# Performance work log

Hardware: AMD Instinct MI355X
Metric: run time of the kernel (lower is better)

## Reference

```python
import jax, jax.numpy as jnp
import numpy as np

B, N = 16, 512            # graphs, atoms per graph
F_DIM, H, D = 128, 64, 16  # feature_dim, hidden_dim, far_source_dim
CUT, GROWTH = 5.0, 2.0
NS, NT = 3, 2
MULT = GROWTH ** NS        # default far_max_radius_multiplier = 8
EMAX = CUT * MULT          # 40.0
TOT = NS + NT              # 5 shells total
SF = D + 3                 # 19 per-shell features
SE_IN = TOT * SF           # 95
EH_IN = 4 * D + SE_IN      # 159
N_RBF = 8
BOUNDS = [(5.0, 10.0), (10.0, 20.0), (20.0, 40.0), (40.0, 80.0), (80.0, float('inf'))]


def ln(x, g, b):
    m = x.mean(-1, keepdims=True)
    v = x.var(-1, keepdims=True)
    return (x - m) / jnp.sqrt(v + 1e-5) * g + b


def setup_inputs() -> dict:
    key = jax.random.key(0)
    ks = jax.random.split(key, 16)
    W = lambda k, i, o: jax.random.normal(k, (i, o), jnp.float32) / np.sqrt(i)
    inp = {}
    inp['x'] = jax.random.normal(ks[0], (B * N, F_DIM), jnp.float32)
    inp['pos'] = jax.random.uniform(ks[1], (B * N, 3), jnp.float32) * 80.0
    inp['batch'] = jnp.repeat(jnp.arange(B, dtype=jnp.int32), N)
    inp['num_graphs'] = B
    inp['in_ln_g'] = jnp.ones(F_DIM); inp['in_ln_b'] = jnp.zeros(F_DIM)
    inp['src_w1'] = W(ks[2], F_DIM, H); inp['src_b1'] = jnp.zeros(H)
    inp['src_w2'] = W(ks[3], H, D);     inp['src_b2'] = jnp.zeros(D)
    inp['src_ln_g'] = jnp.ones(D); inp['src_ln_b'] = jnp.zeros(D)
    inp['se_ln_g'] = jnp.ones(SE_IN); inp['se_ln_b'] = jnp.zeros(SE_IN)
    inp['se_w1'] = W(ks[4], SE_IN, H); inp['se_b1'] = jnp.zeros(H)
    inp['se_w2'] = W(ks[5], H, D);     inp['se_b2'] = jnp.zeros(D)
    inp['eh_ln_g'] = jnp.ones(EH_IN); inp['eh_ln_b'] = jnp.zeros(EH_IN)
    inp['eh_w1'] = W(ks[6], EH_IN, H); inp['eh_b1'] = jnp.zeros(H)
    inp['eh_w2'] = W(ks[7], H, 1);     inp['eh_b2'] = jnp.zeros(1)
    inp['k_screen'] = jnp.float32(-8.0)
    inp['kg_w1'] = W(ks[8], N_RBF + 2, 32); inp['kg_b1'] = jnp.zeros(32)
    inp['kg_w2'] = jnp.zeros((32, 1)); inp['kg_b2'] = jnp.zeros(1)  # zero-init per source
    inp['far_gate'] = jnp.float32(0.2)
    inp['energy_scale'] = jnp.float32(0.0)
    return inp


def reference(x, pos, batch, num_graphs, in_ln_g, in_ln_b, src_w1, src_b1, src_w2, src_b2,
              src_ln_g, src_ln_b, se_ln_g, se_ln_b, se_w1, se_b1, se_w2, se_b2,
              eh_ln_g, eh_ln_b, eh_w1, eh_b1, eh_w2, eh_b2,
              k_screen, kg_w1, kg_b1, kg_w2, kg_b2, far_gate, energy_scale):
    M = x.shape[0]
    n = M // num_graphs
    # per-atom source features
    h = ln(x, in_ln_g, in_ln_b)
    src = jax.nn.silu(h @ src_w1 + src_b1) @ src_w2 + src_b2
    src = ln(src, src_ln_g, src_ln_b)
    # graph-wise neutralization (subtract per-graph mean)
    gsum = jax.ops.segment_sum(src, batch, num_segments=num_graphs)
    cnt = jax.ops.segment_sum(jnp.ones((M, 1), x.dtype), batch, num_segments=num_graphs)
    src = src - (gsum / jnp.maximum(cnt, 1.0))[batch]
    # pairwise distances per graph
    p = pos.reshape(num_graphs, n, 3)
    s = src.reshape(num_graphs, n, D)
    diff = p[:, :, None, :] - p[:, None, :, :]
    d = jnp.sqrt((diff * diff).sum(-1) + 1e-12)  # [B,n,n]
    not_self = ~jnp.eye(n, dtype=bool)[None]
    # physical kernel with learned RBF gate
    screening = jax.nn.softplus(k_screen)
    base = jnp.exp(-screening * d) / jnp.maximum(d, 1e-6)
    centers = jnp.linspace(CUT, EMAX, N_RBF)
    spacing = (EMAX - CUT) / (N_RBF - 1)
    gamma = 1.0 / (spacing * spacing)
    dc = d[..., None]
    rbf = jnp.exp(-gamma * (dc - centers) ** 2)
    gin = jnp.concatenate([dc / CUT, dc / EMAX, rbf], -1)
    gate = 1.0 + jnp.tanh(jax.nn.silu(gin @ kg_w1 + kg_b1) @ kg_w2 + kg_b2)[..., 0]
    ker = base * gate
    # shell statistics: kernel-weighted mean source, count, mean_r, rms_r per shell
    feats = []
    for lo, up in BOUNDS:
        m = (d >= lo) & not_self
        if np.isfinite(up):
            m = m & (d < up)
        mf = m.astype(x.dtype)
        c = mf.sum(-1)
        denom = jnp.maximum(c, 1.0)
        mean = jnp.einsum('bij,bjc->bic', ker * mf, s) / denom[..., None]
        mr = (mf * d).sum(-1) / denom
        rr = jnp.sqrt((mf * d * d).sum(-1) / denom + 1e-12)
        feats.append(jnp.concatenate([mean, c[..., None], mr[..., None], rr[..., None]], -1))
    shell = jnp.concatenate(feats, -1).reshape(M, SE_IN)  # [M, 95]
    emb = jax.nn.silu(ln(shell, se_ln_g, se_ln_b) @ se_w1 + se_b1) @ se_w2 + se_b2
    ein = jnp.concatenate([src, emb, src * emb, src - emb, shell], -1)  # [M, 159]
    pa = (jax.nn.silu(ln(ein, eh_ln_g, eh_ln_b) @ eh_w1 + eh_b1) @ eh_w2 + eh_b2)[..., 0]
    pa = pa * jnp.tanh(far_gate) * jnp.exp(energy_scale)
    return jax.ops.segment_sum(pa, batch, num_segments=num_graphs)  # per-graph energies [B]
```

## Files before the change

kernel.cpp:

```cpp
#include <hip/hip_runtime.h>
#include <hip/hip_bf16.h>
#include <math.h>

#define B_G   16
#define N_A   512
#define M_AT  8192
#define FD    128
#define HD    64
#define DD    16
#define SEIN  95
#define EHIN  159
#define NLUT  1024
#define DMAXF 140.0f

__device__ __forceinline__ float silu_f(float z) { return z / (1.f + __expf(-z)); }

__global__ __launch_bounds__(256) void k_lut2(
    const float* __restrict__ k_screen,
    const float* __restrict__ kg_w1, const float* __restrict__ kg_b1,
    const float* __restrict__ kg_w2, const float* __restrict__ kg_b2,
    float2* __restrict__ lut, float* __restrict__ out) {
  int t = threadIdx.x;
  if (blockIdx.x == 0 && t < B_G) out[t] = 0.f;

  __shared__ float w1l[320], b1l[32], w2l[32];
  for (int idx = t; idx < 320; idx += 256) w1l[idx] = kg_w1[idx];
  if (t < 32) { b1l[t] = kg_b1[t]; w2l[t] = kg_w2[t]; }
  __syncthreads();

  int i = blockIdx.x * 256 + t;
  if (i >= NLUT) return;
  float step = DMAXF / (float)(NLUT - 1);
  float ksv = k_screen[0];
  float screening = fmaxf(ksv, 0.f) + log1pf(expf(-fabsf(ksv)));
  float b2v = kg_b2[0];
  float vals[2];
#pragma unroll
  for (int e = 0; e < 2; ++e) {
    int ii = min(i + e, NLUT - 1);
    float d = (float)ii * step;
    float base = expf(-screening * d) / fmaxf(d, 1e-6f);
    float gin[10];
    gin[0] = d * (1.f / 5.0f);
    gin[1] = d * (1.f / 40.0f);
#pragma unroll
    for (int kk = 0; kk < 8; ++kk) {
      float u = d - (5.0f + 5.0f * (float)kk);
      gin[2 + kk] = expf(-(1.f / 25.f) * u * u);
    }
    float accv = 0.f;
    for (int h = 0; h < 32; ++h) {
      float z = b1l[h];
#pragma unroll
      for (int kk = 0; kk < 10; ++kk) z += gin[kk] * w1l[kk * 32 + h];
      accv += silu_f(z) * w2l[h];
    }
    accv += b2v;
    vals[e] = base * (1.f + tanhf(accv));
  }
  lut[i] = make_float2(vals[0], vals[1] - vals[0]);
}

__global__ __launch_bounds__(128) void k_src(
    const float* __restrict__ x,
    const float* __restrict__ g, const float* __restrict__ bb,
    const float* __restrict__ w1, const float* __restrict__ b1,
    const float* __restrict__ w2, const float* __restrict__ b2,
    const float* __restrict__ lng, const float* __restrict__ lnb,
    float* __restrict__ srcout) {
  int t = threadIdx.x, wave = t >> 6, lane = t & 63;
  __shared__ __align__(16) float w1s[FD * HD];
  __shared__ __align__(16) float w2s[HD * DD];
  __shared__ __align__(16) float xnsA[2][FD][16];
  __shared__ __align__(16) float hbA[2][HD][16];

  for (int idx = t; idx < FD * HD / 4; idx += 128)
    ((float4*)w1s)[idx] = ((const float4*)w1)[idx];
  for (int idx = t; idx < HD * DD / 4; idx += 128)
    ((float4*)w2s)[idx] = ((const float4*)w2)[idx];

  int aBase = blockIdx.x * 32 + wave * 16;
  int al = lane & 15, part = lane >> 4;

  float xr[32];
  const float4* xp = (const float4*)(x + (size_t)(aBase + al) * FD + part * 32);
#pragma unroll
  for (int i = 0; i < 8; ++i) {
    float4 v = xp[i];
    xr[i*4] = v.x; xr[i*4+1] = v.y; xr[i*4+2] = v.z; xr[i*4+3] = v.w;
  }
  float s = 0.f;
#pragma unroll
  for (int i = 0; i < 32; ++i) s += xr[i];
  s += __shfl_xor(s, 16); s += __shfl_xor(s, 32);
  float m = s * (1.f / 128.f);
  float v2 = 0.f;
#pragma unroll
  for (int i = 0; i < 32; ++i) { float d = xr[i] - m; v2 += d * d; }
  v2 += __shfl_xor(v2, 16); v2 += __shfl_xor(v2, 32);
  float inv = rsqrtf(v2 * (1.f / 128.f) + 1e-5f);
#pragma unroll
  for (int i = 0; i < 32; ++i) {
    int k = part * 32 + i;
    xnsA[wave][k][al] = (xr[i] - m) * inv * g[k] + bb[k];
  }
  __syncthreads();

  int h0 = al * 4, a0 = part * 4;
  float acc[4][4] = {};
#pragma unroll 4
  for (int k = 0; k < FD; ++k) {
    float4 wv = *(const float4*)&w1s[k * HD + h0];
    float4 xa = *(const float4*)&xnsA[wave][k][a0];
    acc[0][0] += wv.x * xa.x; acc[0][1] += wv.x * xa.y; acc[0][2] += wv.x * xa.z; acc[0][3] += wv.x * xa.w;
    acc[1][0] += wv.y * xa.x; acc[1][1] += wv.y * xa.y; acc[1][2] += wv.y * xa.z; acc[1][3] += wv.y * xa.w;
    acc[2][0] += wv.z * xa.x; acc[2][1] += wv.z * xa.y; acc[2][2] += wv.z * xa.z; acc[2][3] += wv.z * xa.w;
    acc[3][0] += wv.w * xa.x; acc[3][1] += wv.w * xa.y; acc[3][2] += wv.w * xa.z; acc[3][3] += wv.w * xa.w;
  }
#pragma unroll
  for (int i = 0; i < 4; ++i) {
    float bh = b1[h0 + i];
    float4 o;
    o.x = silu_f(acc[i][0] + bh); o.y = silu_f(acc[i][1] + bh);
    o.z = silu_f(acc[i][2] + bh); o.w = silu_f(acc[i][3] + bh);
    *(float4*)&hbA[wave][h0 + i][a0] = o;
  }
  __syncthreads();

  float acc2[4] = {};
#pragma unroll 4
  for (int h = 0; h < HD; ++h) {
    float wv = w2s[h * DD + al];
    float4 hv = *(const float4*)&hbA[wave][h][a0];
    acc2[0] += wv * hv.x; acc2[1] += wv * hv.y; acc2[2] += wv * hv.z; acc2[3] += wv * hv.w;
  }
  float b2c = b2[al], lgc = lng[al], lbc = lnb[al];
#pragma unroll
  for (int j = 0; j < 4; ++j) {
    float val = acc2[j] + b2c;
    float sm = val;
    sm += __shfl_xor(sm, 1); sm += __shfl_xor(sm, 2); sm += __shfl_xor(sm, 4); sm += __shfl_xor(sm, 8);
    float mm = sm * (1.f / 16.f);
    float dv = val - mm;
    float vv = dv * dv;
    vv += __shfl_xor(vv, 1); vv += __shfl_xor(vv, 2); vv += __shfl_xor(vv, 4); vv += __shfl_xor(vv, 8);
    float iv = rsqrtf(vv * (1.f / 16.f) + 1e-5f);
    srcout[(size_t)(aBase + a0 + j) * DD + al] = dv * iv * lgc + lbc;
  }
}

__global__ __launch_bounds__(256) void k_center(float* __restrict__ src) {
  int gph = blockIdx.x, t = threadIdx.x;
  float4* s4 = (float4*)(src + (size_t)gph * N_A * DD);
  float4 acc = make_float4(0.f, 0.f, 0.f, 0.f);
#pragma unroll
  for (int i = 0; i < 8; ++i) {
    float4 v = s4[t + 256 * i];
    acc.x += v.x; acc.y += v.y; acc.z += v.z; acc.w += v.w;
  }
  __shared__ float4 red[256];
  red[t] = acc;
  __syncthreads();
  if (t < 64) {
    float4 a = red[t], b = red[t + 64], c = red[t + 128], d = red[t + 192];
    a.x += b.x + c.x + d.x; a.y += b.y + c.y + d.y;
    a.z += b.z + c.z + d.z; a.w += b.w + c.w + d.w;
    red[t] = a;
  }
  __syncthreads();
  if (t < 16) {
    float4 a = red[t], b = red[t + 16], c = red[t + 32], d = red[t + 48];
    a.x += b.x + c.x + d.x; a.y += b.y + c.y + d.y;
    a.z += b.z + c.z + d.z; a.w += b.w + c.w + d.w;
    red[t] = a;
  }
  __syncthreads();
  if (t < 4) {
    float4 a = red[t], b = red[t + 4], c = red[t + 8], d = red[t + 12];
    a.x = (a.x + b.x + c.x + d.x) * (1.f / 512.f);
    a.y = (a.y + b.y + c.y + d.y) * (1.f / 512.f);
    a.z = (a.z + b.z + c.z + d.z) * (1.f / 512.f);
    a.w = (a.w + b.w + c.w + d.w) * (1.f / 512.f);
    red[t] = a;
  }
  __syncthreads();
  float4 mv = red[t & 3];
#pragma unroll
  for (int i = 0; i < 8; ++i) {
    int idx = t + 256 * i;
    float4 v = s4[idx];
    v.x -= mv.x; v.y -= mv.y; v.z -= mv.z; v.w -= mv.w;
    s4[idx] = v;
  }
}

__global__ __launch_bounds__(256) void k_pairs(
    const float* __restrict__ pos, const float* __restrict__ src,
    const float2* __restrict__ lut, float* __restrict__ shell) {
  int gph = blockIdx.x >> 7;
  int blk = blockIdx.x & 127;
  int t = threadIdx.x, wave = t >> 6, lane = t & 63;
  int i_local = blk * 4 + wave;

  __shared__ __align__(16) float sp[N_A * 3];
  __shared__ __align__(16) float ss[N_A * DD];
  __shared__ __align__(16) float2 luts[NLUT];
  __shared__ __align__(16) float wb[4][N_A];
  __shared__ unsigned char tbs[4][N_A];

  for (int idx = t; idx < N_A * 3 / 4; idx += 256)
    ((float4*)sp)[idx] = ((const float4*)(pos + (size_t)gph * N_A * 3))[idx];
  for (int idx = t; idx < N_A * DD / 4; idx += 256)
    ((float4*)ss)[idx] = ((const float4*)(src + (size_t)gph * N_A * DD))[idx];
  for (int idx = t; idx < NLUT / 2; idx += 256)
    ((float4*)luts)[idx] = ((const float4*)lut)[idx];
  __syncthreads();

  float px = sp[i_local * 3], py = sp[i_local * 3 + 1], pz = sp[i_local * 3 + 2];
  float cnt[5] = {0,0,0,0,0}, sd[5] = {0,0,0,0,0}, sdd[5] = {0,0,0,0,0};
  const float lscale = (float)(NLUT - 1) / DMAXF;

#pragma unroll
  for (int it = 0; it < 8; ++it) {
    int jv = lane + it * 64;
    float dx = px - sp[jv * 3], dy = py - sp[jv * 3 + 1], dz = pz - sp[jv * 3 + 2];
    float d2 = dx * dx + dy * dy + dz * dz + 1e-12f;
    float d = sqrtf(d2);
    bool valid = (jv != i_local) && (d >= 5.0f);
    int tq = (d >= 10.f) + (d >= 20.f) + (d >= 40.f) + (d >= 80.f);
    float xq = d * lscale;
    int i0 = min((int)xq, NLUT - 2);
    float f = xq - (float)i0;
    float2 L = luts[i0];
    float w = valid ? (L.x + L.y * f) : 0.f;
    wb[wave][jv] = w;
    tbs[wave][jv] = (unsigned char)tq;
    float dm = valid ? d : 0.f;
    float ddm = valid ? d * d : 0.f;
    float cm = valid ? 1.f : 0.f;
#pragma unroll
    for (int q = 0; q < 5; ++q) {
      bool mq = (tq == q);
      cnt[q] += mq ? cm : 0.f;
      sd[q]  += mq ? dm : 0.f;
      sdd[q] += mq ? ddm : 0.f;
    }
  }
#pragma unroll
  for (int q = 0; q < 5; ++q) {
#pragma unroll
    for (int o = 32; o > 0; o >>= 1) {
      cnt[q] += __shfl_xor(cnt[q], o);
      sd[q]  += __shfl_xor(sd[q], o);
      sdd[q] += __shfl_xor(sdd[q], o);
    }
  }
  __syncthreads();

  int jlow = lane & 15, cq = lane >> 4;
  float accq[5][4] = {};
  const float* ssb = &ss[jlow * DD + cq * 4];
  const float* wbb = &wb[wave][jlow];
  const unsigned char* tbb = &tbs[wave][jlow];
#pragma unroll
  for (int jj = 0; jj < 32; ++jj) {
    float4 sv = *(const float4*)(ssb + jj * 256);
    float w = wbb[jj * 16];
    int tq = tbb[jj * 16];
    float w0 = (tq == 0) ? w : 0.f;
    float w1_ = (tq == 1) ? w : 0.f;
    float w2_ = (tq == 2) ? w : 0.f;
    float w3_ = (tq == 3) ? w : 0.f;
    float w4_ = (tq == 4) ? w : 0.f;
    accq[0][0] += w0 * sv.x; accq[0][1] += w0 * sv.y; accq[0][2] += w0 * sv.z; accq[0][3] += w0 * sv.w;
    accq[1][0] += w1_ * sv.x; accq[1][1] += w1_ * sv.y; accq[1][2] += w1_ * sv.z; accq[1][3] += w1_ * sv.w;
    accq[2][0] += w2_ * sv.x; accq[2][1] += w2_ * sv.y; accq[2][2] += w2_ * sv.z; accq[2][3] += w2_ * sv.w;
    accq[3][0] += w3_ * sv.x; accq[3][1] += w3_ * sv.y; accq[3][2] += w3_ * sv.z; accq[3][3] += w3_ * sv.w;
    accq[4][0] += w4_ * sv.x; accq[4][1] += w4_ * sv.y; accq[4][2] += w4_ * sv.z; accq[4][3] += w4_ * sv.w;
  }
#pragma unroll
  for (int q = 0; q < 5; ++q)
#pragma unroll
    for (int i = 0; i < 4; ++i) {
      float v = accq[q][i];
      v += __shfl_xor(v, 1); v += __shfl_xor(v, 2); v += __shfl_xor(v, 4); v += __shfl_xor(v, 8);
      accq[q][i] = v;
    }

  float* shp = shell + (size_t)(gph * N_A + i_local) * SEIN;
  if (jlow == 0) {
#pragma unroll
    for (int q = 0; q < 5; ++q)
#pragma unroll
      for (int i = 0; i < 4; ++i)
        shp[q * 19 + cq * 4 + i] = accq[q][i] / fmaxf(cnt[q], 1.f);
  }
  if (lane < 5) {
    int q = lane;
    float denom = fmaxf(cnt[q], 1.f);
    shp[q * 19 + 16] = cnt[q];
    shp[q * 19 + 17] = sd[q] / denom;
    shp[q * 19 + 18] = sqrtf(sdd[q] / denom + 1e-12f);
  }
}

__global__ __launch_bounds__(128) void k_tail_a(
    const float* __restrict__ shell,
    const float* __restrict__ se_ln_g, const float* __restrict__ se_ln_b,
    const float* __restrict__ se_w1, const float* __restrict__ se_b1,
    const float* __restrict__ se_w2, const float* __restrict__ se_b2,
    float* __restrict__ emb) {
  int t = threadIdx.x, wave = t >> 6, lane = t & 63;
  __shared__ __align__(16) float w1s[SEIN * HD];
  __shared__ __align__(16) float w2s[HD * DD];
  __shared__ __align__(16) float shnA[2][SEIN][16];
  __shared__ __align__(16) float hbA[2][HD][16];

  for (int idx = t; idx < SEIN * HD / 4; idx += 128)
    ((float4*)w1s)[idx] = ((const float4*)se_w1)[idx];
  for (int idx = t; idx < HD * DD / 4; idx += 128)
    ((float4*)w2s)[idx] = ((const float4*)se_w2)[idx];

  int aB = blockIdx.x * 32;
  const float* shg = shell + (size_t)aB * SEIN;
  for (int idx = t; idx < 32 * SEIN; idx += 128) {
    unsigned a_loc = ((unsigned)idx * 690u) >> 16;
    int kk = idx - (int)a_loc * SEIN;
    shnA[a_loc >> 4][kk][a_loc & 15] = shg[idx];
  }
  __syncthreads();

  int al = lane & 15, part = lane >> 4;
  float s1 = 0.f, sq = 0.f;
  for (int i = 0; i < 24; ++i) {
    int k = part * 24 + i;
    if (k < SEIN) { float v = shnA[wave][k][al]; s1 += v; sq += v * v; }
  }
  s1 += __shfl_xor(s1, 16); s1 += __shfl_xor(s1, 32);
  sq += __shfl_xor(sq, 16); sq += __shfl_xor(sq, 32);
  float m = s1 * (1.f / (float)SEIN);
  float var = sq * (1.f / (float)SEIN) - m * m;
  float inv = rsqrtf(var + 1e-5f);
  for (int i = 0; i < 24; ++i) {
    int k = part * 24 + i;
    if (k < SEIN)
      shnA[wave][k][al] = (shnA[wave][k][al] - m) * inv * se_ln_g[k] + se_ln_b[k];
  }
  __syncthreads();

  int h0 = al * 4, a0 = part * 4;
  float acc[4][4] = {};
#pragma unroll 5
  for (int k = 0; k < SEIN; ++k) {
    float4 wv = *(const float4*)&w1s[k * HD + h0];
    float4 xa = *(const float4*)&shnA[wave][k][a0];
    acc[0][0] += wv.x * xa.x; acc[0][1] += wv.x * xa.y; acc[0][2] += wv.x * xa.z; acc[0][3] += wv.x * xa.w;
    acc[1][0] += wv.y * xa.x; acc[1][1] += wv.y * xa.y; acc[1][2] += wv.y * xa.z; acc[1][3] += wv.y * xa.w;
    acc[2][0] += wv.z * xa.x; acc[2][1] += wv.z * xa.y; acc[2][2] += wv.z * xa.z; acc[2][3] += wv.z * xa.w;
    acc[3][0] += wv.w * xa.x; acc[3][1] += wv.w * xa.y; acc[3][2] += wv.w * xa.z; acc[3][3] += wv.w * xa.w;
  }
#pragma unroll
  for (int i = 0; i < 4; ++i) {
    float bh = se_b1[h0 + i];
    float4 o;
    o.x = silu_f(acc[i][0] + bh); o.y = silu_f(acc[i][1] + bh);
    o.z = silu_f(acc[i][2] + bh); o.w = silu_f(acc[i][3] + bh);
    *(float4*)&hbA[wave][h0 + i][a0] = o;
  }
  __syncthreads();

  float acc2[4] = {};
#pragma unroll 4
  for (int h = 0; h < HD; ++h) {
    float wv = w2s[h * DD + al];
    float4 hv = *(const float4*)&hbA[wave][h][a0];
    acc2[0] += wv * hv.x; acc2[1] += wv * hv.y; acc2[2] += wv * hv.z; acc2[3] += wv * hv.w;
  }
  float b2c = se_b2[al];
#pragma unroll
  for (int j = 0; j < 4; ++j)
    emb[(size_t)(aB + wave * 16 + a0 + j) * DD + al] = acc2[j] + b2c;
}

__global__ __launch_bounds__(128) void k_tail_b(
    const float* __restrict__ src, const float* __restrict__ embp,
    const float* __restrict__ shell,
    const float* __restrict__ eh_ln_g, const float* __restrict__ eh_ln_b,
    const float* __restrict__ eh_w1, const float* __restrict__ eh_b1,
    const float* __restrict__ eh_w2, const float* __restrict__ eh_b2,
    const float* __restrict__ far_gate, const float* __restrict__ energy_scale,
    float* __restrict__ out) {
  int t = threadIdx.x, wave = t >> 6, lane = t & 63;
  __shared__ __align__(16) float w1s[EHIN * HD];
  __shared__ __align__(16) float einA[2][EHIN][16];
  __shared__ float redv[2][4];

  for (int idx = t; idx < EHIN * HD / 4; idx += 128)
    ((float4*)w1s)[idx] = ((const float4*)eh_w1)[idx];

  int aB = blockIdx.x * 32;
  int gph = aB >> 9;

  for (int idx = t; idx < 32 * DD; idx += 128) {
    int a_loc = idx >> 4, k = idx & 15;
    float sv = src[(size_t)aB * DD + idx];
    float ev = embp[(size_t)aB * DD + idx];
    int wv_ = a_loc >> 4, ac = a_loc & 15;
    einA[wv_][k][ac] = sv;
    einA[wv_][16 + k][ac] = ev;
    einA[wv_][32 + k][ac] = sv * ev;
    einA[wv_][48 + k][ac] = sv - ev;
  }
  const float* shg = shell + (size_t)aB * SEIN;
  for (int idx = t; idx < 32 * SEIN; idx += 128) {
    unsigned a_loc = ((unsigned)idx * 690u) >> 16;
    int kk = idx - (int)a_loc * SEIN;
    einA[a_loc >> 4][64 + kk][a_loc & 15] = shg[idx];
  }
  __syncthreads();

  int al = lane & 15, part = lane >> 4;
  float s1 = 0.f, sq = 0.f;
  for (int i = 0; i < 40; ++i) {
    int k = part * 40 + i;
    if (k < EHIN) { float v = einA[wave][k][al]; s1 += v; sq += v * v; }
  }
  s1 += __shfl_xor(s1, 16); s1 += __shfl_xor(s1, 32);
  sq += __shfl_xor(sq, 16); sq += __shfl_xor(sq, 32);
  float m = s1 * (1.f / (float)EHIN);
  float var = sq * (1.f / (float)EHIN) - m * m;
  float inv = rsqrtf(var + 1e-5f);
  for (int i = 0; i < 40; ++i) {
    int k = part * 40 + i;
    if (k < EHIN)
      einA[wave][k][al] = (einA[wave][k][al] - m) * inv * eh_ln_g[k] + eh_ln_b[k];
  }
  __syncthreads();

  int h0 = al * 4, a0 = part * 4;
  float acc[4][4] = {};
#pragma unroll 3
  for (int k = 0; k < EHIN; ++k) {
    float4 wv = *(const float4*)&w1s[k * HD + h0];
    float4 xa = *(const float4*)&einA[wave][k][a0];
    acc[0][0] += wv.x * xa.x; acc[0][1] += wv.x * xa.y; acc[0][2] += wv.x * xa.z; acc[0][3] += wv.x * xa.w;
    acc[1][0] += wv.y * xa.x; acc[1][1] += wv.y * xa.y; acc[1][2] += wv.y * xa.z; acc[1][3] += wv.y * xa.w;
    acc[2][0] += wv.z * xa.x; acc[2][1] += wv.z * xa.y; acc[2][2] += wv.z * xa.z; acc[2][3] += wv.z * xa.w;
    acc[3][0] += wv.w * xa.x; acc[3][1] += wv.w * xa.y; acc[3][2] += wv.w * xa.z; acc[3][3] += wv.w * xa.w;
  }
  float pa[4] = {0.f, 0.f, 0.f, 0.f};
#pragma unroll
  for (int i = 0; i < 4; ++i) {
    float bh = eh_b1[h0 + i];
    float w2v = eh_w2[h0 + i];
#pragma unroll
    for (int j = 0; j < 4; ++j) pa[j] += silu_f(acc[i][j] + bh) * w2v;
  }
#pragma unroll
  for (int j = 0; j < 4; ++j) {
    pa[j] += __shfl_xor(pa[j], 1); pa[j] += __shfl_xor(pa[j], 2);
    pa[j] += __shfl_xor(pa[j], 4); pa[j] += __shfl_xor(pa[j], 8);
  }
  if (al == 0) redv[wave][part] = pa[0] + pa[1] + pa[2] + pa[3] + 4.f * eh_b2[0];
  __syncthreads();
  if (t == 0) {
    float tot = 0.f;
#pragma unroll
    for (int w2_ = 0; w2_ < 2; ++w2_)
#pragma unroll
      for (int p = 0; p < 4; ++p) tot += redv[w2_][p];
    atomicAdd(&out[gph], tot * tanhf(far_gate[0]) * expf(energy_scale[0]));
  }
}

extern "C" void kernel_launch(void* const* d_in, const int* in_sizes, int n_in,
                              void* d_out, int out_size, void* d_ws, size_t ws_size,
                              hipStream_t stream) {
  const float* x         = (const float*)d_in[0];
  const float* pos       = (const float*)d_in[1];
  const float* in_ln_g   = (const float*)d_in[4];
  const float* in_ln_b   = (const float*)d_in[5];
  const float* src_w1    = (const float*)d_in[6];
  const float* src_b1    = (const float*)d_in[7];
  const float* src_w2    = (const float*)d_in[8];
  const float* src_b2    = (const float*)d_in[9];
  const float* src_ln_g  = (const float*)d_in[10];
  const float* src_ln_b  = (const float*)d_in[11];
  const float* se_ln_g   = (const float*)d_in[12];
  const float* se_ln_b   = (const float*)d_in[13];
  const float* se_w1     = (const float*)d_in[14];
  const float* se_b1     = (const float*)d_in[15];
  const float* se_w2     = (const float*)d_in[16];
  const float* se_b2     = (const float*)d_in[17];
  const float* eh_ln_g   = (const float*)d_in[18];
  const float* eh_ln_b   = (const float*)d_in[19];
  const float* eh_w1     = (const float*)d_in[20];
  const float* eh_b1     = (const float*)d_in[21];
  const float* eh_w2     = (const float*)d_in[22];
  const float* eh_b2     = (const float*)d_in[23];
  const float* k_screen  = (const float*)d_in[24];
  const float* kg_w1     = (const float*)d_in[25];
  const float* kg_b1     = (const float*)d_in[26];
  const float* kg_w2     = (const float*)d_in[27];
  const float* kg_b2     = (const float*)d_in[28];
  const float* far_gate  = (const float*)d_in[29];
  const float* en_scale  = (const float*)d_in[30];
  float* out = (float*)d_out;

  float* ws_src   = (float*)d_ws;
  float* ws_shell = ws_src + (size_t)M_AT * DD;
  float* ws_emb   = ws_shell + (size_t)M_AT * SEIN;
  float2* ws_lut  = (float2*)(ws_emb + (size_t)M_AT * DD);

  k_lut2<<<NLUT / 256, 256, 0, stream>>>(k_screen, kg_w1, kg_b1, kg_w2, kg_b2,
                                         ws_lut, out);
  k_src<<<M_AT / 32, 128, 0, stream>>>(x, in_ln_g, in_ln_b, src_w1, src_b1,
                                       src_w2, src_b2, src_ln_g, src_ln_b, ws_src);
  k_center<<<B_G, 256, 0, stream>>>(ws_src);
  k_pairs<<<B_G * (N_A / 4), 256, 0, stream>>>(pos, ws_src, ws_lut, ws_shell);
  k_tail_a<<<M_AT / 32, 128, 0, stream>>>(ws_shell, se_ln_g, se_ln_b,
                                          se_w1, se_b1, se_w2, se_b2, ws_emb);
  k_tail_b<<<M_AT / 32, 128, 0, stream>>>(ws_src, ws_emb, ws_shell,
                                          eh_ln_g, eh_ln_b, eh_w1, eh_b1, eh_w2, eh_b2,
                                          far_gate, en_scale, out);
}
```

Baseline: 221.0 us.

## Fuse six kernels into three and fold mean-centering into downstream sums

Merges the LUT builder into the source-MLP kernel as extra blocks, and replaces the separate centering kernel with per-block partial sums. Consumers subtract the mean algebraically: shell means use a kernel-weight sum times the mean, and the tail subtracts it from src directly. The two tail MLP kernels are fused so the embedding never goes through global memory. Weight staging in LDS is replaced by direct global reads, and the LUT is halved to 512 entries. This cuts launches and intermediate traffic at the cost of LUT interpolation accuracy and some extra per-block reduction work.

```diff
diff --git a/kernel.cpp b/kernel.cpp
--- a/kernel.cpp
+++ b/kernel.cpp
@@ -10,80 +10,73 @@
 #define DD    16
 #define SEIN  95
 #define EHIN  159
-#define NLUT  1024
+#define NLUT  512
 #define DMAXF 140.0f
 
 __device__ __forceinline__ float silu_f(float z) { return z / (1.f + __expf(-z)); }
 
-__global__ __launch_bounds__(256) void k_lut2(
-    const float* __restrict__ k_screen,
-    const float* __restrict__ kg_w1, const float* __restrict__ kg_b1,
-    const float* __restrict__ kg_w2, const float* __restrict__ kg_b2,
-    float2* __restrict__ lut, float* __restrict__ out) {
-  int t = threadIdx.x;
-  if (blockIdx.x == 0 && t < B_G) out[t] = 0.f;
-
-  __shared__ float w1l[320], b1l[32], w2l[32];
-  for (int idx = t; idx < 320; idx += 256) w1l[idx] = kg_w1[idx];
-  if (t < 32) { b1l[t] = kg_b1[t]; w2l[t] = kg_w2[t]; }
-  __syncthreads();
-
-  int i = blockIdx.x * 256 + t;
-  if (i >= NLUT) return;
-  float step = DMAXF / (float)(NLUT - 1);
-  float ksv = k_screen[0];
-  float screening = fmaxf(ksv, 0.f) + log1pf(expf(-fabsf(ksv)));
-  float b2v = kg_b2[0];
-  float vals[2];
-#pragma unroll
-  for (int e = 0; e < 2; ++e) {
-    int ii = min(i + e, NLUT - 1);
-    float d = (float)ii * step;
-    float base = expf(-screening * d) / fmaxf(d, 1e-6f);
-    float gin[10];
-    gin[0] = d * (1.f / 5.0f);
-    gin[1] = d * (1.f / 40.0f);
-#pragma unroll
-    for (int kk = 0; kk < 8; ++kk) {
-      float u = d - (5.0f + 5.0f * (float)kk);
-      gin[2 + kk] = expf(-(1.f / 25.f) * u * u);
-    }
-    float accv = 0.f;
-    for (int h = 0; h < 32; ++h) {
-      float z = b1l[h];
-#pragma unroll
-      for (int kk = 0; kk < 10; ++kk) z += gin[kk] * w1l[kk * 32 + h];
-      accv += silu_f(z) * w2l[h];
-    }
-    accv += b2v;
-    vals[e] = base * (1.f + tanhf(accv));
-  }
-  lut[i] = make_float2(vals[0], vals[1] - vals[0]);
-}
-
-__global__ __launch_bounds__(128) void k_src(
+__global__ __launch_bounds__(128) void k_front(
     const float* __restrict__ x,
     const float* __restrict__ g, const float* __restrict__ bb,
     const float* __restrict__ w1, const float* __restrict__ b1,
     const float* __restrict__ w2, const float* __restrict__ b2,
     const float* __restrict__ lng, const float* __restrict__ lnb,
-    float* __restrict__ srcout) {
-  int t = threadIdx.x, wave = t >> 6, lane = t & 63;
-  __shared__ __align__(16) float w1s[FD * HD];
-  __shared__ __align__(16) float w2s[HD * DD];
+    const float* __restrict__ k_screen,
+    const float* __restrict__ kg_w1, const float* __restrict__ kg_b1,
+    const float* __restrict__ kg_w2, const float* __restrict__ kg_b2,
+    float* __restrict__ srcout, float* __restrict__ partials,
+    float2* __restrict__ lut, float* __restrict__ out) {
+  int t = threadIdx.x;
+
+  if (blockIdx.x >= 256) {
+    int lb = blockIdx.x - 256;
+    __shared__ float w1l[320], b1l[32], w2l[32];
+    if (lb == 0 && t < B_G) out[t] = 0.f;
+    for (int idx = t; idx < 320; idx += 128) w1l[idx] = kg_w1[idx];
+    if (t < 32) { b1l[t] = kg_b1[t]; w2l[t] = kg_w2[t]; }
+    __syncthreads();
+    int i = lb * 128 + t;
+    float step = DMAXF / (float)(NLUT - 1);
+    float ksv = k_screen[0];
+    float screening = fmaxf(ksv, 0.f) + log1pf(expf(-fabsf(ksv)));
+    float b2v = kg_b2[0];
+    float vals[2];
+#pragma unroll
+    for (int e = 0; e < 2; ++e) {
+      int ii = min(i + e, NLUT - 1);
+      float d = (float)ii * step;
+      float base = expf(-screening * d) / fmaxf(d, 1e-6f);
+      float gin[10];
+      gin[0] = d * (1.f / 5.0f);
+      gin[1] = d * (1.f / 40.0f);
+#pragma unroll
+      for (int kk = 0; kk < 8; ++kk) {
+        float u = d - (5.0f + 5.0f * (float)kk);
+        gin[2 + kk] = expf(-(1.f / 25.f) * u * u);
+      }
+      float accv = 0.f;
+      for (int h = 0; h < 32; ++h) {
+        float z = b1l[h];
+#pragma unroll
+        for (int kk = 0; kk < 10; ++kk) z += gin[kk] * w1l[kk * 32 + h];
+        accv += silu_f(z) * w2l[h];
+      }
+      vals[e] = base * (1.f + tanhf(accv + b2v));
+    }
+    lut[i] = make_float2(vals[0], vals[1] - vals[0]);
+    return;
+  }
+
+  int wave = t >> 6, lane = t & 63;
   __shared__ __align__(16) float xnsA[2][FD][16];
   __shared__ __align__(16) float hbA[2][HD][16];
-
-  for (int idx = t; idx < FD * HD / 4; idx += 128)
-    ((float4*)w1s)[idx] = ((const float4*)w1)[idx];
-  for (int idx = t; idx < HD * DD / 4; idx += 128)
-    ((float4*)w2s)[idx] = ((const float4*)w2)[idx];
+  __shared__ float psum[2][16];
 
   int aBase = blockIdx.x * 32 + wave * 16;
-  int al = lane & 15, part = lane >> 4;
+  int al = lane & 15, prt = lane >> 4;
 
   float xr[32];
-  const float4* xp = (const float4*)(x + (size_t)(aBase + al) * FD + part * 32);
+  const float4* xp = (const float4*)(x + (size_t)(aBase + al) * FD + prt * 32);
 #pragma unroll
   for (int i = 0; i < 8; ++i) {
     float4 v = xp[i];
@@ -101,40 +94,44 @@
   float inv = rsqrtf(v2 * (1.f / 128.f) + 1e-5f);
 #pragma unroll
   for (int i = 0; i < 32; ++i) {
-    int k = part * 32 + i;
+    int k = prt * 32 + i;
     xnsA[wave][k][al] = (xr[i] - m) * inv * g[k] + bb[k];
   }
   __syncthreads();
 
-  int h0 = al * 4, a0 = part * 4;
+  int h0 = al * 4, a0 = prt * 4;
   float acc[4][4] = {};
 #pragma unroll 4
   for (int k = 0; k < FD; ++k) {
-    float4 wv = *(const float4*)&w1s[k * HD + h0];
+    float4 wv = ((const float4*)(w1 + (size_t)k * HD))[al];
     float4 xa = *(const float4*)&xnsA[wave][k][a0];
     acc[0][0] += wv.x * xa.x; acc[0][1] += wv.x * xa.y; acc[0][2] += wv.x * xa.z; acc[0][3] += wv.x * xa.w;
     acc[1][0] += wv.y * xa.x; acc[1][1] += wv.y * xa.y; acc[1][2] += wv.y * xa.z; acc[1][3] += wv.y * xa.w;
     acc[2][0] += wv.z * xa.x; acc[2][1] += wv.z * xa.y; acc[2][2] += wv.z * xa.z; acc[2][3] += wv.z * xa.w;
     acc[3][0] += wv.w * xa.x; acc[3][1] += wv.w * xa.y; acc[3][2] += wv.w * xa.z; acc[3][3] += wv.w * xa.w;
   }
-#pragma unroll
-  for (int i = 0; i < 4; ++i) {
-    float bh = b1[h0 + i];
-    float4 o;
-    o.x = silu_f(acc[i][0] + bh); o.y = silu_f(acc[i][1] + bh);
-    o.z = silu_f(acc[i][2] + bh); o.w = silu_f(acc[i][3] + bh);
-    *(float4*)&hbA[wave][h0 + i][a0] = o;
+  {
+    float4 bv = ((const float4*)b1)[al];
+    float bh[4] = {bv.x, bv.y, bv.z, bv.w};
+#pragma unroll
+    for (int i = 0; i < 4; ++i) {
+      float4 o;
+      o.x = silu_f(acc[i][0] + bh[i]); o.y = silu_f(acc[i][1] + bh[i]);
+      o.z = silu_f(acc[i][2] + bh[i]); o.w = silu_f(acc[i][3] + bh[i]);
+      *(float4*)&hbA[wave][h0 + i][a0] = o;
+    }
   }
   __syncthreads();
 
   float acc2[4] = {};
 #pragma unroll 4
   for (int h = 0; h < HD; ++h) {
-    float wv = w2s[h * DD + al];
+    float wv = w2[h * DD + al];
     float4 hv = *(const float4*)&hbA[wave][h][a0];
     acc2[0] += wv * hv.x; acc2[1] += wv * hv.y; acc2[2] += wv * hv.z; acc2[3] += wv * hv.w;
   }
   float b2c = b2[al], lgc = lng[al], lbc = lnb[al];
+  float lsum = 0.f;
 #pragma unroll
   for (int j = 0; j < 4; ++j) {
     float val = acc2[j] + b2c;
@@ -145,58 +142,20 @@
     float vv = dv * dv;
     vv += __shfl_xor(vv, 1); vv += __shfl_xor(vv, 2); vv += __shfl_xor(vv, 4); vv += __shfl_xor(vv, 8);
     float iv = rsqrtf(vv * (1.f / 16.f) + 1e-5f);
-    srcout[(size_t)(aBase + a0 + j) * DD + al] = dv * iv * lgc + lbc;
-  }
-}
-
-__global__ __launch_bounds__(256) void k_center(float* __restrict__ src) {
-  int gph = blockIdx.x, t = threadIdx.x;
-  float4* s4 = (float4*)(src + (size_t)gph * N_A * DD);
-  float4 acc = make_float4(0.f, 0.f, 0.f, 0.f);
-#pragma unroll
-  for (int i = 0; i < 8; ++i) {
-    float4 v = s4[t + 256 * i];
-    acc.x += v.x; acc.y += v.y; acc.z += v.z; acc.w += v.w;
-  }
-  __shared__ float4 red[256];
-  red[t] = acc;
-  __syncthreads();
-  if (t < 64) {
-    float4 a = red[t], b = red[t + 64], c = red[t + 128], d = red[t + 192];
-    a.x += b.x + c.x + d.x; a.y += b.y + c.y + d.y;
-    a.z += b.z + c.z + d.z; a.w += b.w + c.w + d.w;
-    red[t] = a;
-  }
-  __syncthreads();
-  if (t < 16) {
-    float4 a = red[t], b = red[t + 16], c = red[t + 32], d = red[t + 48];
-    a.x += b.x + c.x + d.x; a.y += b.y + c.y + d.y;
-    a.z += b.z + c.z + d.z; a.w += b.w + c.w + d.w;
-    red[t] = a;
-  }
-  __syncthreads();
-  if (t < 4) {
-    float4 a = red[t], b = red[t + 4], c = red[t + 8], d = red[t + 12];
-    a.x = (a.x + b.x + c.x + d.x) * (1.f / 512.f);
-    a.y = (a.y + b.y + c.y + d.y) * (1.f / 512.f);
-    a.z = (a.z + b.z + c.z + d.z) * (1.f / 512.f);
-    a.w = (a.w + b.w + c.w + d.w) * (1.f / 512.f);
-    red[t] = a;
-  }
-  __syncthreads();
-  float4 mv = red[t & 3];
-#pragma unroll
-  for (int i = 0; i < 8; ++i) {
-    int idx = t + 256 * i;
-    float4 v = s4[idx];
-    v.x -= mv.x; v.y -= mv.y; v.z -= mv.z; v.w -= mv.w;
-    s4[idx] = v;
-  }
+    float ov = dv * iv * lgc + lbc;
+    srcout[(size_t)(aBase + a0 + j) * DD + al] = ov;
+    lsum += ov;
+  }
+  lsum += __shfl_xor(lsum, 16); lsum += __shfl_xor(lsum, 32);
+  if (lane < 16) psum[wave][al] = lsum;
+  __syncthreads();
+  if (t < 16) partials[(size_t)blockIdx.x * 16 + t] = psum[0][t] + psum[1][t];
 }
 
 __global__ __launch_bounds__(256) void k_pairs(
     const float* __restrict__ pos, const float* __restrict__ src,
-    const float2* __restrict__ lut, float* __restrict__ shell) {
+    const float2* __restrict__ lut, const float* __restrict__ partials,
+    float* __restrict__ shell) {
   int gph = blockIdx.x >> 7;
   int blk = blockIdx.x & 127;
   int t = threadIdx.x, wave = t >> 6, lane = t & 63;
@@ -207,17 +166,26 @@
   __shared__ __align__(16) float2 luts[NLUT];
   __shared__ __align__(16) float wb[4][N_A];
   __shared__ unsigned char tbs[4][N_A];
+  __shared__ float smean[16];
 
   for (int idx = t; idx < N_A * 3 / 4; idx += 256)
     ((float4*)sp)[idx] = ((const float4*)(pos + (size_t)gph * N_A * 3))[idx];
   for (int idx = t; idx < N_A * DD / 4; idx += 256)
     ((float4*)ss)[idx] = ((const float4*)(src + (size_t)gph * N_A * DD))[idx];
-  for (int idx = t; idx < NLUT / 2; idx += 256)
-    ((float4*)luts)[idx] = ((const float4*)lut)[idx];
+  if (t < NLUT / 2) ((float4*)luts)[t] = ((const float4*)lut)[t];
+  if (t < 64) {
+    int c = t & 15, grp = t >> 4;
+    float sm = 0.f;
+#pragma unroll
+    for (int k = 0; k < 4; ++k)
+      sm += partials[(size_t)(gph * 16 + grp * 4 + k) * 16 + c];
+    sm += __shfl_xor(sm, 16); sm += __shfl_xor(sm, 32);
+    if (t < 16) smean[c] = sm * (1.f / 512.f);
+  }
   __syncthreads();
 
   float px = sp[i_local * 3], py = sp[i_local * 3 + 1], pz = sp[i_local * 3 + 2];
-  float cnt[5] = {0,0,0,0,0}, sd[5] = {0,0,0,0,0}, sdd[5] = {0,0,0,0,0};
+  float cnt[5] = {0,0,0,0,0}, sd[5] = {0,0,0,0,0}, sdd[5] = {0,0,0,0,0}, sw[5] = {0,0,0,0,0};
   const float lscale = (float)(NLUT - 1) / DMAXF;
 
 #pragma unroll
@@ -244,6 +212,7 @@
       cnt[q] += mq ? cm : 0.f;
       sd[q]  += mq ? dm : 0.f;
       sdd[q] += mq ? ddm : 0.f;
+      sw[q]  += mq ? w : 0.f;
     }
   }
 #pragma unroll
@@ -253,6 +222,7 @@
       cnt[q] += __shfl_xor(cnt[q], o);
       sd[q]  += __shfl_xor(sd[q], o);
       sdd[q] += __shfl_xor(sdd[q], o);
+      sw[q]  += __shfl_xor(sw[q], o);
     }
   }
   __syncthreads();
@@ -290,10 +260,14 @@
   float* shp = shell + (size_t)(gph * N_A + i_local) * SEIN;
   if (jlow == 0) {
 #pragma unroll
-    for (int q = 0; q < 5; ++q)
-#pragma unroll
-      for (int i = 0; i < 4; ++i)
-        shp[q * 19 + cq * 4 + i] = accq[q][i] / fmaxf(cnt[q], 1.f);
+    for (int q = 0; q < 5; ++q) {
+      float denom = fmaxf(cnt[q], 1.f);
+#pragma unroll
+      for (int i = 0; i < 4; ++i) {
+        int c = cq * 4 + i;
+        shp[q * 19 + c] = (accq[q][i] - smean[c] * sw[q]) / denom;
+      }
+    }
   }
   if (lane < 5) {
     int q = lane;
@@ -304,113 +278,37 @@
   }
 }
 
-__global__ __launch_bounds__(128) void k_tail_a(
-    const float* __restrict__ shell,
+__global__ __launch_bounds__(128) void k_tail(
+    const float* __restrict__ src, const float* __restrict__ shell,
+    const float* __restrict__ partials,
     const float* __restrict__ se_ln_g, const float* __restrict__ se_ln_b,
     const float* __restrict__ se_w1, const float* __restrict__ se_b1,
     const float* __restrict__ se_w2, const float* __restrict__ se_b2,
-    float* __restrict__ emb) {
-  int t = threadIdx.x, wave = t >> 6, lane = t & 63;
-  __shared__ __align__(16) float w1s[SEIN * HD];
-  __shared__ __align__(16) float w2s[HD * DD];
-  __shared__ __align__(16) float shnA[2][SEIN][16];
-  __shared__ __align__(16) float hbA[2][HD][16];
-
-  for (int idx = t; idx < SEIN * HD / 4; idx += 128)
-    ((float4*)w1s)[idx] = ((const float4*)se_w1)[idx];
-  for (int idx = t; idx < HD * DD / 4; idx += 128)
-    ((float4*)w2s)[idx] = ((const float4*)se_w2)[idx];
-
-  int aB = blockIdx.x * 32;
-  const float* shg = shell + (size_t)aB * SEIN;
-  for (int idx = t; idx < 32 * SEIN; idx += 128) {
-    unsigned a_loc = ((unsigned)idx * 690u) >> 16;
-    int kk = idx - (int)a_loc * SEIN;
-    shnA[a_loc >> 4][kk][a_loc & 15] = shg[idx];
-  }
-  __syncthreads();
-
-  int al = lane & 15, part = lane >> 4;
-  float s1 = 0.f, sq = 0.f;
-  for (int i = 0; i < 24; ++i) {
-    int k = part * 24 + i;
-    if (k < SEIN) { float v = shnA[wave][k][al]; s1 += v; sq += v * v; }
-  }
-  s1 += __shfl_xor(s1, 16); s1 += __shfl_xor(s1, 32);
-  sq += __shfl_xor(sq, 16); sq += __shfl_xor(sq, 32);
-  float m = s1 * (1.f / (float)SEIN);
-  float var = sq * (1.f / (float)SEIN) - m * m;
-  float inv = rsqrtf(var + 1e-5f);
-  for (int i = 0; i < 24; ++i) {
-    int k = part * 24 + i;
-    if (k < SEIN)
-      shnA[wave][k][al] = (shnA[wave][k][al] - m) * inv * se_ln_g[k] + se_ln_b[k];
-  }
-  __syncthreads();
-
-  int h0 = al * 4, a0 = part * 4;
-  float acc[4][4] = {};
-#pragma unroll 5
-  for (int k = 0; k < SEIN; ++k) {
-    float4 wv = *(const float4*)&w1s[k * HD + h0];
-    float4 xa = *(const float4*)&shnA[wave][k][a0];
-    acc[0][0] += wv.x * xa.x; acc[0][1] += wv.x * xa.y; acc[0][2] += wv.x * xa.z; acc[0][3] += wv.x * xa.w;
-    acc[1][0] += wv.y * xa.x; acc[1][1] += wv.y * xa.y; acc[1][2] += wv.y * xa.z; acc[1][3] += wv.y * xa.w;
-    acc[2][0] += wv.z * xa.x; acc[2][1] += wv.z * xa.y; acc[2][2] += wv.z * xa.z; acc[2][3] += wv.z * xa.w;
-    acc[3][0] += wv.w * xa.x; acc[3][1] += wv.w * xa.y; acc[3][2] += wv.w * xa.z; acc[3][3] += wv.w * xa.w;
-  }
-#pragma unroll
-  for (int i = 0; i < 4; ++i) {
-    float bh = se_b1[h0 + i];
-    float4 o;
-    o.x = silu_f(acc[i][0] + bh); o.y = silu_f(acc[i][1] + bh);
-    o.z = silu_f(acc[i][2] + bh); o.w = silu_f(acc[i][3] + bh);
-    *(float4*)&hbA[wave][h0 + i][a0] = o;
-  }
-  __syncthreads();
-
-  float acc2[4] = {};
-#pragma unroll 4
-  for (int h = 0; h < HD; ++h) {
-    float wv = w2s[h * DD + al];
-    float4 hv = *(const float4*)&hbA[wave][h][a0];
-    acc2[0] += wv * hv.x; acc2[1] += wv * hv.y; acc2[2] += wv * hv.z; acc2[3] += wv * hv.w;
-  }
-  float b2c = se_b2[al];
-#pragma unroll
-  for (int j = 0; j < 4; ++j)
-    emb[(size_t)(aB + wave * 16 + a0 + j) * DD + al] = acc2[j] + b2c;
-}
-
-__global__ __launch_bounds__(128) void k_tail_b(
-    const float* __restrict__ src, const float* __restrict__ embp,
-    const float* __restrict__ shell,
     const float* __restrict__ eh_ln_g, const float* __restrict__ eh_ln_b,
     const float* __restrict__ eh_w1, const float* __restrict__ eh_b1,
     const float* __restrict__ eh_w2, const float* __restrict__ eh_b2,
     const float* __restrict__ far_gate, const float* __restrict__ energy_scale,
     float* __restrict__ out) {
   int t = threadIdx.x, wave = t >> 6, lane = t & 63;
-  __shared__ __align__(16) float w1s[EHIN * HD];
   __shared__ __align__(16) float einA[2][EHIN][16];
+  __shared__ __align__(16) float shnA[2][SEIN][16];
+  __shared__ __align__(16) float hbA[2][HD][16];
+  __shared__ float smean[16];
   __shared__ float redv[2][4];
-
-  for (int idx = t; idx < EHIN * HD / 4; idx += 128)
-    ((float4*)w1s)[idx] = ((const float4*)eh_w1)[idx];
 
   int aB = blockIdx.x * 32;
   int gph = aB >> 9;
 
-  for (int idx = t; idx < 32 * DD; idx += 128) {
-    int a_loc = idx >> 4, k = idx & 15;
-    float sv = src[(size_t)aB * DD + idx];
-    float ev = embp[(size_t)aB * DD + idx];
-    int wv_ = a_loc >> 4, ac = a_loc & 15;
-    einA[wv_][k][ac] = sv;
-    einA[wv_][16 + k][ac] = ev;
-    einA[wv_][32 + k][ac] = sv * ev;
-    einA[wv_][48 + k][ac] = sv - ev;
-  }
+  if (t < 64) {
+    int c = t & 15, grp = t >> 4;
+    float sm = 0.f;
+#pragma unroll
+    for (int k = 0; k < 4; ++k)
+      sm += partials[(size_t)(gph * 16 + grp * 4 + k) * 16 + c];
+    sm += __shfl_xor(sm, 16); sm += __shfl_xor(sm, 32);
+    if (t < 16) smean[c] = sm * (1.f / 512.f);
+  }
+
   const float* shg = shell + (size_t)aB * SEIN;
   for (int idx = t; idx < 32 * SEIN; idx += 128) {
     unsigned a_loc = ((unsigned)idx * 690u) >> 16;
@@ -419,56 +317,125 @@
   }
   __syncthreads();
 
-  int al = lane & 15, part = lane >> 4;
-  float s1 = 0.f, sq = 0.f;
-  for (int i = 0; i < 40; ++i) {
-    int k = part * 40 + i;
-    if (k < EHIN) { float v = einA[wave][k][al]; s1 += v; sq += v * v; }
-  }
-  s1 += __shfl_xor(s1, 16); s1 += __shfl_xor(s1, 32);
-  sq += __shfl_xor(sq, 16); sq += __shfl_xor(sq, 32);
-  float m = s1 * (1.f / (float)EHIN);
-  float var = sq * (1.f / (float)EHIN) - m * m;
-  float inv = rsqrtf(var + 1e-5f);
-  for (int i = 0; i < 40; ++i) {
-    int k = part * 40 + i;
-    if (k < EHIN)
-      einA[wave][k][al] = (einA[wave][k][al] - m) * inv * eh_ln_g[k] + eh_ln_b[k];
-  }
-  __syncthreads();
-
-  int h0 = al * 4, a0 = part * 4;
-  float acc[4][4] = {};
+  int al = lane & 15, prt = lane >> 4;
+  {
+    float s1 = 0.f, sq = 0.f;
+    for (int i = 0; i < 24; ++i) {
+      int k = prt * 24 + i;
+      if (k < SEIN) { float v = einA[wave][64 + k][al]; s1 += v; sq += v * v; }
+    }
+    s1 += __shfl_xor(s1, 16); s1 += __shfl_xor(s1, 32);
+    sq += __shfl_xor(sq, 16); sq += __shfl_xor(sq, 32);
+    float m = s1 * (1.f / (float)SEIN);
+    float var = sq * (1.f / (float)SEIN) - m * m;
+    float inv = rsqrtf(var + 1e-5f);
+    for (int i = 0; i < 24; ++i) {
+      int k = prt * 24 + i;
+      if (k < SEIN)
+        shnA[wave][k][al] = (einA[wave][64 + k][al] - m) * inv * se_ln_g[k] + se_ln_b[k];
+    }
+  }
+  __syncthreads();
+
+  int h0 = al * 4, a0 = prt * 4;
+  {
+    float acc[4][4] = {};
+#pragma unroll 5
+    for (int k = 0; k < SEIN; ++k) {
+      float4 wv = ((const float4*)(se_w1 + (size_t)k * HD))[al];
+      float4 xa = *(const float4*)&shnA[wave][k][a0];
+      acc[0][0] += wv.x * xa.x; acc[0][1] += wv.x * xa.y; acc[0][2] += wv.x * xa.z; acc[0][3] += wv.x * xa.w;
+      acc[1][0] += wv.y * xa.x; acc[1][1] += wv.y * xa.y; acc[1][2] += wv.y * xa.z; acc[1][3] += wv.y * xa.w;
+      acc[2][0] += wv.z * xa.x; acc[2][1] += wv.z * xa.y; acc[2][2] += wv.z * xa.z; acc[2][3] += wv.z * xa.w;
+      acc[3][0] += wv.w * xa.x; acc[3][1] += wv.w * xa.y; acc[3][2] += wv.w * xa.z; acc[3][3] += wv.w * xa.w;
+    }
+    float4 bv = ((const float4*)se_b1)[al];
+    float bh[4] = {bv.x, bv.y, bv.z, bv.w};
+#pragma unroll
+    for (int i = 0; i < 4; ++i) {
+      float4 o;
+      o.x = silu_f(acc[i][0] + bh[i]); o.y = silu_f(acc[i][1] + bh[i]);
+      o.z = silu_f(acc[i][2] + bh[i]); o.w = silu_f(acc[i][3] + bh[i]);
+      *(float4*)&hbA[wave][h0 + i][a0] = o;
+    }
+  }
+  __syncthreads();
+
+  {
+    float acc2[4] = {};
+#pragma unroll 4
+    for (int h = 0; h < HD; ++h) {
+      float wv = se_w2[h * DD + al];
+      float4 hv = *(const float4*)&hbA[wave][h][a0];
+      acc2[0] += wv * hv.x; acc2[1] += wv * hv.y; acc2[2] += wv * hv.z; acc2[3] += wv * hv.w;
+    }
+    float b2c = se_b2[al], smc = smean[al];
+    int aW = aB + wave * 16;
+#pragma unroll
+    for (int j = 0; j < 4; ++j) {
+      float ev = acc2[j] + b2c;
+      float sv = src[(size_t)(aW + a0 + j) * DD + al] - smc;
+      einA[wave][al][a0 + j] = sv;
+      einA[wave][16 + al][a0 + j] = ev;
+      einA[wave][32 + al][a0 + j] = sv * ev;
+      einA[wave][48 + al][a0 + j] = sv - ev;
+    }
+  }
+  __syncthreads();
+
+  {
+    float s1 = 0.f, sq = 0.f;
+    for (int i = 0; i < 40; ++i) {
+      int k = prt * 40 + i;
+      if (k < EHIN) { float v = einA[wave][k][al]; s1 += v; sq += v * v; }
+    }
+    s1 += __shfl_xor(s1, 16); s1 += __shfl_xor(s1, 32);
+    sq += __shfl_xor(sq, 16); sq += __shfl_xor(sq, 32);
+    float m = s1 * (1.f / (float)EHIN);
+    float var = sq * (1.f / (float)EHIN) - m * m;
+    float inv = rsqrtf(var + 1e-5f);
+    for (int i = 0; i < 40; ++i) {
+      int k = prt * 40 + i;
+      if (k < EHIN)
+        einA[wave][k][al] = (einA[wave][k][al] - m) * inv * eh_ln_g[k] + eh_ln_b[k];
+    }
+  }
+  __syncthreads();
+
+  {
+    float acc[4][4] = {};
 #pragma unroll 3
-  for (int k = 0; k < EHIN; ++k) {
-    float4 wv = *(const float4*)&w1s[k * HD + h0];
-    float4 xa = *(const float4*)&einA[wave][k][a0];
-    acc[0][0] += wv.x * xa.x; acc[0][1] += wv.x * xa.y; acc[0][2] += wv.x * xa.z; acc[0][3] += wv.x * xa.w;
-    acc[1][0] += wv.y * xa.x; acc[1][1] += wv.y * xa.y; acc[1][2] += wv.y * xa.z; acc[1][3] += wv.y * xa.w;
-    acc[2][0] += wv.z * xa.x; acc[2][1] += wv.z * xa.y; acc[2][2] += wv.z * xa.z; acc[2][3] += wv.z * xa.w;
-    acc[3][0] += wv.w * xa.x; acc[3][1] += wv.w * xa.y; acc[3][2] += wv.w * xa.z; acc[3][3] += wv.w * xa.w;
-  }
-  float pa[4] = {0.f, 0.f, 0.f, 0.f};
-#pragma unroll
-  for (int i = 0; i < 4; ++i) {
-    float bh = eh_b1[h0 + i];
-    float w2v = eh_w2[h0 + i];
-#pragma unroll
-    for (int j = 0; j < 4; ++j) pa[j] += silu_f(acc[i][j] + bh) * w2v;
-  }
-#pragma unroll
-  for (int j = 0; j < 4; ++j) {
-    pa[j] += __shfl_xor(pa[j], 1); pa[j] += __shfl_xor(pa[j], 2);
-    pa[j] += __shfl_xor(pa[j], 4); pa[j] += __shfl_xor(pa[j], 8);
-  }
-  if (al == 0) redv[wave][part] = pa[0] + pa[1] + pa[2] + pa[3] + 4.f * eh_b2[0];
+    for (int k = 0; k < EHIN; ++k) {
+      float4 wv = ((const float4*)(eh_w1 + (size_t)k * HD))[al];
+      float4 xa = *(const float4*)&einA[wave][k][a0];
+      acc[0][0] += wv.x * xa.x; acc[0][1] += wv.x * xa.y; acc[0][2] += wv.x * xa.z; acc[0][3] += wv.x * xa.w;
+      acc[1][0] += wv.y * xa.x; acc[1][1] += wv.y * xa.y; acc[1][2] += wv.y * xa.z; acc[1][3] += wv.y * xa.w;
+      acc[2][0] += wv.z * xa.x; acc[2][1] += wv.z * xa.y; acc[2][2] += wv.z * xa.z; acc[2][3] += wv.z * xa.w;
+      acc[3][0] += wv.w * xa.x; acc[3][1] += wv.w * xa.y; acc[3][2] += wv.w * xa.z; acc[3][3] += wv.w * xa.w;
+    }
+    float4 b1v = ((const float4*)eh_b1)[al];
+    float4 w2v = ((const float4*)eh_w2)[al];
+    float bh[4] = {b1v.x, b1v.y, b1v.z, b1v.w};
+    float wh[4] = {w2v.x, w2v.y, w2v.z, w2v.w};
+    float pa[4] = {0.f, 0.f, 0.f, 0.f};
+#pragma unroll
+    for (int i = 0; i < 4; ++i)
+#pragma unroll
+      for (int j = 0; j < 4; ++j) pa[j] += silu_f(acc[i][j] + bh[i]) * wh[i];
+#pragma unroll
+    for (int j = 0; j < 4; ++j) {
+      pa[j] += __shfl_xor(pa[j], 1); pa[j] += __shfl_xor(pa[j], 2);
+      pa[j] += __shfl_xor(pa[j], 4); pa[j] += __shfl_xor(pa[j], 8);
+    }
+    if (al == 0) redv[wave][prt] = pa[0] + pa[1] + pa[2] + pa[3] + 4.f * eh_b2[0];
+  }
   __syncthreads();
   if (t == 0) {
     float tot = 0.f;
 #pragma unroll
-    for (int w2_ = 0; w2_ < 2; ++w2_)
-#pragma unroll
-      for (int p = 0; p < 4; ++p) tot += redv[w2_][p];
+    for (int w_ = 0; w_ < 2; ++w_)
+#pragma unroll
+      for (int p = 0; p < 4; ++p) tot += redv[w_][p];
     atomicAdd(&out[gph], tot * tanhf(far_gate[0]) * expf(energy_scale[0]));
   }
 }
@@ -509,18 +476,16 @@
 
   float* ws_src   = (float*)d_ws;
   float* ws_shell = ws_src + (size_t)M_AT * DD;
-  float* ws_emb   = ws_shell + (size_t)M_AT * SEIN;
-  float2* ws_lut  = (float2*)(ws_emb + (size_t)M_AT * DD);
-
-  k_lut2<<<NLUT / 256, 256, 0, stream>>>(k_screen, kg_w1, kg_b1, kg_w2, kg_b2,
-                                         ws_lut, out);
-  k_src<<<M_AT / 32, 128, 0, stream>>>(x, in_ln_g, in_ln_b, src_w1, src_b1,
-                                       src_w2, src_b2, src_ln_g, src_ln_b, ws_src);
-  k_center<<<B_G, 256, 0, stream>>>(ws_src);
-  k_pairs<<<B_G * (N_A / 4), 256, 0, stream>>>(pos, ws_src, ws_lut, ws_shell);
-  k_tail_a<<<M_AT / 32, 128, 0, stream>>>(ws_shell, se_ln_g, se_ln_b,
-                                          se_w1, se_b1, se_w2, se_b2, ws_emb);
-  k_tail_b<<<M_AT / 32, 128, 0, stream>>>(ws_src, ws_emb, ws_shell,
-                                          eh_ln_g, eh_ln_b, eh_w1, eh_b1, eh_w2, eh_b2,
-                                          far_gate, en_scale, out);
+  float* ws_part  = ws_shell + (size_t)M_AT * SEIN;
+  float2* ws_lut  = (float2*)(ws_part + 256 * 16);
+
+  k_front<<<260, 128, 0, stream>>>(x, in_ln_g, in_ln_b, src_w1, src_b1,
+                                   src_w2, src_b2, src_ln_g, src_ln_b,
+                                   k_screen, kg_w1, kg_b1, kg_w2, kg_b2,
+                                   ws_src, ws_part, ws_lut, out);
+  k_pairs<<<B_G * (N_A / 4), 256, 0, stream>>>(pos, ws_src, ws_lut, ws_part, ws_shell);
+  k_tail<<<M_AT / 32, 128, 0, stream>>>(ws_src, ws_shell, ws_part,
+                                        se_ln_g, se_ln_b, se_w1, se_b1, se_w2, se_b2,
+                                        eh_ln_g, eh_ln_b, eh_w1, eh_b1, eh_w2, eh_b2,
+                                        far_gate, en_scale, out);
 }
```

Result: faster. 209.3 us (-5.3%).
